# Performance work log

Measured on AMD Instinct MI355X. Metric: run time of the kernel, lower is better.

## Reference

```python
import jax, jax.numpy as jnp
import numpy as np

B, S, D, H = 4, 2048, 512, 512

def setup_inputs() -> dict:
    key = jax.random.key(0)
    ks = jax.random.split(key, 9)
    sc_d = 1.0 / np.sqrt(D)
    sc_s = 1.0 / np.sqrt(S)
    return {
        "x": jax.random.normal(ks[0], (B, S, D), dtype=jnp.float32),
        "Wq": jax.random.normal(ks[1], (D, H), dtype=jnp.float32) * sc_d,
        "bq": jnp.zeros((H,), dtype=jnp.float32),
        "Wk": jax.random.normal(ks[2], (D, H), dtype=jnp.float32) * sc_d,
        "bk": jnp.zeros((H,), dtype=jnp.float32),
        "Wv": jax.random.normal(ks[3], (D, H), dtype=jnp.float32) * sc_d,
        "bv": jnp.zeros((H,), dtype=jnp.float32),
        "Wd": jax.random.normal(ks[4], (S, H), dtype=jnp.float32) * sc_s,
        "bd": jnp.zeros((H,), dtype=jnp.float32),
    }

def reference(x, Wq, bq, Wk, bk, Wv, bv, Wd, bd):
    # q, k, v: [B, S, H]
    q = x @ Wq + bq
    k = x @ Wk + bk
    v = x @ Wv + bv
    # raw scores: [B, S, S]
    qk = jnp.einsum('bsh,bth->bst', q, k)
    # Dense+sigmoid over the last (seqlen) axis: [B, S, H]
    dense_out = jax.nn.sigmoid(qk @ Wd + bd)
    # value weights: [B, S, S]
    vw = jnp.einsum('bsh,bth->bst', dense_out, v)
    # out: [B, S, D]
    return jnp.einsum('bst,btd->bsd', vw, x)
```

## Files before the change

kernel.cpp:

```cpp
#include <hip/hip_runtime.h>
#include <hip/hip_bf16.h>
#include <stdint.h>

#define BB 4
#define SS 2048
#define DD 512
#define HH 512

typedef __attribute__((ext_vector_type(8))) short short8;
typedef __attribute__((ext_vector_type(4))) float floatx4;

typedef __attribute__((address_space(3))) uint32_t lds_u32_t;
typedef const __attribute__((address_space(1))) uint32_t glb_u32_t;

__device__ __forceinline__ void gload_lds16(const void* g, void* l) {
  __builtin_amdgcn_global_load_lds((glb_u32_t*)g, (lds_u32_t*)l, 16, 0, 0);
}

__device__ __forceinline__ short f2bf(float f) {
  __hip_bfloat16 h = __float2bfloat16(f);
  return __builtin_bit_cast(short, h);
}

__device__ __forceinline__ float bf2f(short s) {
  uint32_t u = ((uint32_t)(uint16_t)s) << 16;
  return __builtin_bit_cast(float, u);
}

template <int BM, int EPI>
__device__ __forceinline__ void gemm_core(
    const short* __restrict__ A, const short* __restrict__ Bm,
    void* __restrict__ Cm, long c_base, const float* __restrict__ bias, int K,
    int lda, int ldb, int ldc, long row0, long col0) {
  constexpr int BK = 32;
  constexpr int MF = BM / 32;
  __shared__ short As[BM * BK];
  __shared__ short Bs[128 * BK];

  const short* Ab = A + row0 * lda;
  const short* Bb = Bm + col0 * ldb;

  const int t = threadIdx.x;
  const int lane = t & 63;
  const int wid = t >> 6;
  const int wr = wid >> 1, wc = wid & 1;
  const int r16 = lane & 15;
  const int kc = (lane >> 4) * 8;

  const int st_row = t >> 2;
  const int st_k = (t & 3) * 8;

  floatx4 acc[MF][4];
#pragma unroll
  for (int i = 0; i < MF; i++)
#pragma unroll
    for (int j = 0; j < 4; j++) acc[i][j] = (floatx4)0.f;

  for (int k0 = 0; k0 < K; k0 += BK) {
#pragma unroll
    for (int i = 0; i < BM / 64; i++)
      gload_lds16(Ab + (long)(i * 64 + st_row) * lda + k0 + st_k,
                  &As[(i * 64 + st_row) * BK + st_k]);
#pragma unroll
    for (int i = 0; i < 2; i++)
      gload_lds16(Bb + (long)(i * 64 + st_row) * ldb + k0 + st_k,
                  &Bs[(i * 64 + st_row) * BK + st_k]);
    __syncthreads();

    short8 af[MF], bfr[4];
#pragma unroll
    for (int i = 0; i < MF; i++)
      af[i] = *(const short8*)&As[(wr * (BM / 2) + i * 16 + r16) * BK + kc];
#pragma unroll
    for (int j = 0; j < 4; j++)
      bfr[j] = *(const short8*)&Bs[(wc * 64 + j * 16 + r16) * BK + kc];
#pragma unroll
    for (int i = 0; i < MF; i++)
#pragma unroll
      for (int j = 0; j < 4; j++)
        acc[i][j] = __builtin_amdgcn_mfma_f32_16x16x32_bf16(af[i], bfr[j],
                                                            acc[i][j], 0, 0, 0);
    __syncthreads();
  }

#pragma unroll
  for (int i = 0; i < MF; i++) {
    const long rbase = row0 + wr * (BM / 2) + i * 16 + (lane >> 4) * 4;
#pragma unroll
    for (int j = 0; j < 4; j++) {
      const long col = col0 + wc * 64 + j * 16 + r16;
      float bv = 0.f;
      if (EPI == 1 || EPI == 2) bv = bias[col];
#pragma unroll
      for (int rg = 0; rg < 4; rg++) {
        float v = acc[i][j][rg];
        if (EPI == 1) v += bv;
        if (EPI == 2) v = 1.f / (1.f + __expf(-(v + bv)));
        const long idx = c_base + (rbase + rg) * ldc + col;
        if (EPI == 3)
          ((float*)Cm)[idx] = v;
        else
          ((__hip_bfloat16*)Cm)[idx] = __float2bfloat16(v);
      }
    }
  }
}

template <int BM, int EPI>
__global__ __launch_bounds__(256) void gemm_bt(
    const short* __restrict__ A, const short* __restrict__ Bm,
    void* __restrict__ Cm, const float* __restrict__ bias, int K, int lda,
    int ldb, int ldc, long sA, long sB, long sC) {
  const int bz = blockIdx.z;
  gemm_core<BM, EPI>(A + bz * sA, Bm + bz * sB, Cm, bz * sC, bias, K, lda, ldb,
                     ldc, (long)blockIdx.x * BM, (long)blockIdx.y * 128);
}

__global__ __launch_bounds__(256) void gemm_dual_split(
    const short* __restrict__ WdT, const short* __restrict__ kT,
    short* __restrict__ partM2, const short* __restrict__ xT,
    const short* __restrict__ vT, short* __restrict__ partM3) {
  const int bz = blockIdx.z;
  const int tb = bz >> 2, sp = bz & 3;
  const int task = tb >> 2, b = tb & 3;
  const short* A = (task ? xT + (long)b * HH * SS : WdT) + sp * 512;
  const short* B = (task ? vT : kT) + (long)b * HH * SS + sp * 512;
  short* C = (task ? partM3 : partM2) + ((long)(tb & 3) * 4 + sp) * HH * HH;
  gemm_core<128, 0>(A, B, C, 0, nullptr, 512, SS, SS, HH,
                    (long)blockIdx.x * 128, (long)blockIdx.y * 128);
}

__global__ __launch_bounds__(256) void reduce_part(
    const short* __restrict__ partM2, const short* __restrict__ partM3,
    short* __restrict__ M2, short* __restrict__ M3t) {
  const int z = blockIdx.z;
  const int b = z & 3;
  const short* src = (z < 4 ? partM2 : partM3) + (long)b * 4 * HH * HH;
  short* dst = (z < 4 ? M2 : M3t) + (long)b * HH * HH;
  const long i = ((long)blockIdx.x * 256 + threadIdx.x) * 8;
  float s[8];
#pragma unroll
  for (int j = 0; j < 8; j++) s[j] = 0.f;
#pragma unroll
  for (int sp = 0; sp < 4; sp++) {
    short8 v = *(const short8*)&src[(long)sp * HH * HH + i];
#pragma unroll
    for (int j = 0; j < 8; j++) s[j] += bf2f(v[j]);
  }
  short o[8];
#pragma unroll
  for (int j = 0; j < 8; j++) o[j] = f2bf(s[j]);
  *(short8*)&dst[i] = *(short8*)o;
}

__global__ void tr_x(const float* __restrict__ x, short* __restrict__ xb,
                     short* __restrict__ xT) {
  __shared__ float tile[32][33];
  const long b = blockIdx.z;
  const float* in = x + b * SS * DD;
  const int c0 = blockIdx.x * 32, r0 = blockIdx.y * 32;
  const int tx = threadIdx.x, ty = threadIdx.y;
#pragma unroll
  for (int i = 0; i < 32; i += 8) {
    float v = in[(long)(r0 + ty + i) * DD + c0 + tx];
    tile[ty + i][tx] = v;
    xb[(b * SS + r0 + ty + i) * DD + c0 + tx] = f2bf(v);
  }
  __syncthreads();
#pragma unroll
  for (int i = 0; i < 32; i += 8)
    xT[(b * DD + c0 + ty + i) * SS + r0 + tx] = f2bf(tile[tx][ty + i]);
}

__global__ void tr_cvt(const float* __restrict__ in, short* __restrict__ out,
                       int R, int C) {
  __shared__ float tile[32][33];
  const int c0 = blockIdx.x * 32, r0 = blockIdx.y * 32;
  const int tx = threadIdx.x, ty = threadIdx.y;
#pragma unroll
  for (int i = 0; i < 32; i += 8)
    tile[ty + i][tx] = in[(long)(r0 + ty + i) * C + c0 + tx];
  __syncthreads();
#pragma unroll
  for (int i = 0; i < 32; i += 8)
    out[(long)(c0 + ty + i) * R + r0 + tx] = f2bf(tile[tx][ty + i]);
}

__global__ void trW3(const float* __restrict__ Wq, const float* __restrict__ Wk,
                     const float* __restrict__ Wv, short* __restrict__ WT) {
  __shared__ float tile[32][33];
  const int z = blockIdx.z;
  const float* in = z == 0 ? Wq : (z == 1 ? Wk : Wv);
  short* out = WT + (long)z * HH * DD;
  const int c0 = blockIdx.x * 32, r0 = blockIdx.y * 32;
  const int tx = threadIdx.x, ty = threadIdx.y;
#pragma unroll
  for (int i = 0; i < 32; i += 8)
    tile[ty + i][tx] = in[(long)(r0 + ty + i) * HH + c0 + tx];
  __syncthreads();
#pragma unroll
  for (int i = 0; i < 32; i += 8)
    out[(long)(c0 + ty + i) * DD + r0 + tx] = f2bf(tile[tx][ty + i]);
}

__global__ void tr_kv(const short* __restrict__ qkv, short* __restrict__ kT,
                      short* __restrict__ vT) {
  __shared__ short tile[32][34];
  const int z = blockIdx.z;
  const int which = z >> 2, b = z & 3;
  const short* in = qkv + (long)b * SS * (3 * HH) + (1 + which) * HH;
  short* out = (which ? vT : kT) + (long)b * HH * SS;
  const int c0 = blockIdx.x * 32, r0 = blockIdx.y * 32;
  const int tx = threadIdx.x, ty = threadIdx.y;
#pragma unroll
  for (int i = 0; i < 32; i += 8)
    tile[ty + i][tx] = in[(long)(r0 + ty + i) * (3 * HH) + c0 + tx];
  __syncthreads();
#pragma unroll
  for (int i = 0; i < 32; i += 8)
    out[(long)(c0 + ty + i) * SS + r0 + tx] = tile[tx][ty + i];
}

__global__ void bias_cat(const float* __restrict__ bq,
                         const float* __restrict__ bk,
                         const float* __restrict__ bv,
                         float* __restrict__ bcat) {
  int i = blockIdx.x * blockDim.x + threadIdx.x;
  if (i < 512)
    bcat[i] = bq[i];
  else if (i < 1024)
    bcat[i] = bk[i - 512];
  else if (i < 1536)
    bcat[i] = bv[i - 1024];
}

extern "C" void kernel_launch(void* const* d_in, const int* in_sizes, int n_in,
                              void* d_out, int out_size, void* d_ws,
                              size_t ws_size, hipStream_t stream) {
  (void)in_sizes;
  (void)n_in;
  (void)out_size;
  (void)ws_size;
  const float* x = (const float*)d_in[0];
  const float* Wq = (const float*)d_in[1];
  const float* bq = (const float*)d_in[2];
  const float* Wk = (const float*)d_in[3];
  const float* bk = (const float*)d_in[4];
  const float* Wv = (const float*)d_in[5];
  const float* bv = (const float*)d_in[6];
  const float* Wd = (const float*)d_in[7];
  const float* bd = (const float*)d_in[8];

  char* w = (char*)d_ws;
  auto alloc = [&](size_t bytes) {
    char* p = w;
    w += (bytes + 255) & ~(size_t)255;
    return p;
  };
  short* xb = (short*)alloc((size_t)BB * SS * DD * 2);
  short* xT = (short*)alloc((size_t)BB * DD * SS * 2);
  short* WT = (short*)alloc((size_t)3 * HH * DD * 2);
  short* WdT = (short*)alloc((size_t)HH * SS * 2);
  float* bcat = (float*)alloc((size_t)3 * HH * 4);
  short* qkv = (short*)alloc((size_t)BB * SS * 3 * HH * 2);
  short* kT = (short*)alloc((size_t)BB * HH * SS * 2);
  short* vT = (short*)alloc((size_t)BB * HH * SS * 2);
  short* M2 = (short*)alloc((size_t)BB * HH * HH * 2);
  short* M3t = (short*)alloc((size_t)BB * DD * HH * 2);
  short* partM3 = (short*)alloc((size_t)BB * 4 * HH * HH * 2);
  short* partM2 = xb;
  short* dense = xb;

  dim3 tb(32, 8);
  tr_x<<<dim3(DD / 32, SS / 32, BB), tb, 0, stream>>>(x, xb, xT);
  trW3<<<dim3(HH / 32, DD / 32, 3), tb, 0, stream>>>(Wq, Wk, Wv, WT);
  tr_cvt<<<dim3(HH / 32, SS / 32, 1), tb, 0, stream>>>(Wd, WdT, SS, HH);
  bias_cat<<<6, 256, 0, stream>>>(bq, bk, bv, bcat);

  gemm_bt<128, 1><<<dim3(BB * SS / 128, 1536 / 128, 1), 256, 0, stream>>>(
      xb, WT, qkv, bcat, DD, DD, DD, 3 * HH, 0, 0, 0);
  tr_kv<<<dim3(HH / 32, SS / 32, 8), tb, 0, stream>>>(qkv, kT, vT);
  gemm_dual_split<<<dim3(4, 4, 32), 256, 0, stream>>>(WdT, kT, partM2, xT, vT,
                                                      partM3);
  reduce_part<<<dim3(128, 1, 8), 256, 0, stream>>>(partM2, partM3, M2, M3t);
  gemm_bt<64, 2><<<dim3(SS / 64, HH / 128, BB), 256, 0, stream>>>(
      qkv, M2, dense, bd, HH, 3 * HH, HH, HH, (long)SS * 3 * HH, (long)HH * HH,
      (long)SS * HH);
  gemm_bt<64, 3><<<dim3(SS / 64, DD / 128, BB), 256, 0, stream>>>(
      dense, M3t, d_out, nullptr, HH, HH, HH, DD, (long)SS * HH, (long)DD * HH,
      (long)SS * DD);
}
```

Measured before the change: 100.1 us.

## Fuse K/V transpose into QKV GEMM epilogue and merge weight prep kernels

The QKV projection now writes q row-major and writes k and v directly in transposed layout from the GEMM epilogue, which removes the separate tr_kv pass and the round trip through the qkv buffer. The three weight and bias preparation kernels are merged into one launch. The split-K GEMM switches to BM=64 tiles with twice as many blocks, and the aliased scratch buffers become separate allocations. The transposed epilogue stores are 8-byte strided writes, which may coalesce worse than the original row stores.

New measurement: 90.72 us. 9.4% less time.

```diff
diff --git a/kernel.cpp b/kernel.cpp
--- a/kernel.cpp
+++ b/kernel.cpp
@@ -27,18 +27,15 @@
   return __builtin_bit_cast(float, u);
 }
 
-template <int BM, int EPI>
-__device__ __forceinline__ void gemm_core(
-    const short* __restrict__ A, const short* __restrict__ Bm,
-    void* __restrict__ Cm, long c_base, const float* __restrict__ bias, int K,
-    int lda, int ldb, int ldc, long row0, long col0) {
+template <int BM>
+__device__ __forceinline__ void gemm_mainloop(const short* __restrict__ Ab,
+                                              const short* __restrict__ Bb,
+                                              int lda, int ldb, int K,
+                                              floatx4 (&acc)[BM / 32][4]) {
   constexpr int BK = 32;
   constexpr int MF = BM / 32;
   __shared__ short As[BM * BK];
   __shared__ short Bs[128 * BK];
-
-  const short* Ab = A + row0 * lda;
-  const short* Bb = Bm + col0 * ldb;
 
   const int t = threadIdx.x;
   const int lane = t & 63;
@@ -50,7 +47,6 @@
   const int st_row = t >> 2;
   const int st_k = (t & 3) * 8;
 
-  floatx4 acc[MF][4];
 #pragma unroll
   for (int i = 0; i < MF; i++)
 #pragma unroll
@@ -82,19 +78,28 @@
                                                             acc[i][j], 0, 0, 0);
     __syncthreads();
   }
-
-#pragma unroll
-  for (int i = 0; i < MF; i++) {
+}
+
+template <int BM, int EPI>
+__device__ __forceinline__ void epilogue_std(floatx4 (&acc)[BM / 32][4],
+                                             void* __restrict__ Cm, long c_base,
+                                             const float* __restrict__ bias,
+                                             int ldc, long row0, long col0) {
+  const int lane = threadIdx.x & 63;
+  const int wid = threadIdx.x >> 6;
+  const int wr = wid >> 1, wc = wid & 1;
+  const int r16 = lane & 15;
+#pragma unroll
+  for (int i = 0; i < BM / 32; i++) {
     const long rbase = row0 + wr * (BM / 2) + i * 16 + (lane >> 4) * 4;
 #pragma unroll
     for (int j = 0; j < 4; j++) {
       const long col = col0 + wc * 64 + j * 16 + r16;
       float bv = 0.f;
-      if (EPI == 1 || EPI == 2) bv = bias[col];
+      if (EPI == 2) bv = bias[col];
 #pragma unroll
       for (int rg = 0; rg < 4; rg++) {
         float v = acc[i][j][rg];
-        if (EPI == 1) v += bv;
         if (EPI == 2) v = 1.f / (1.f + __expf(-(v + bv)));
         const long idx = c_base + (rbase + rg) * ldc + col;
         if (EPI == 3)
@@ -112,8 +117,51 @@
     void* __restrict__ Cm, const float* __restrict__ bias, int K, int lda,
     int ldb, int ldc, long sA, long sB, long sC) {
   const int bz = blockIdx.z;
-  gemm_core<BM, EPI>(A + bz * sA, Bm + bz * sB, Cm, bz * sC, bias, K, lda, ldb,
-                     ldc, (long)blockIdx.x * BM, (long)blockIdx.y * 128);
+  floatx4 acc[BM / 32][4];
+  const long row0 = (long)blockIdx.x * BM, col0 = (long)blockIdx.y * 128;
+  gemm_mainloop<BM>(A + bz * sA + row0 * lda, Bm + bz * sB + col0 * ldb, lda,
+                    ldb, K, acc);
+  epilogue_std<BM, EPI>(acc, Cm, bz * sC, bias, ldc, row0, col0);
+}
+
+__global__ __launch_bounds__(256) void gemm_qkv(
+    const short* __restrict__ xb, const short* __restrict__ WT,
+    const float* __restrict__ bcat, short* __restrict__ q,
+    short* __restrict__ kT, short* __restrict__ vT) {
+  floatx4 acc[4][4];
+  const long row0 = (long)blockIdx.x * 128;
+  const int y = blockIdx.y;
+  gemm_mainloop<128>(xb + row0 * DD, WT + (long)y * 128 * DD, DD, DD, DD, acc);
+
+  const int lane = threadIdx.x & 63;
+  const int wid = threadIdx.x >> 6;
+  const int wr = wid >> 1, wc = wid & 1;
+  const int r16 = lane & 15;
+  const int hi4 = (lane >> 4) * 4;
+  const int mode = y >> 2;
+  const int b = (int)(row0 >> 11);
+  const int sblk = (int)(row0 & 2047);
+  short* tp = (mode == 1) ? kT : vT;
+#pragma unroll
+  for (int i = 0; i < 4; i++) {
+    const int s0 = sblk + wr * 64 + i * 16 + hi4;
+#pragma unroll
+    for (int j = 0; j < 4; j++) {
+      const int colg = y * 128 + wc * 64 + j * 16 + r16;
+      const float bv = bcat[colg];
+      short o[4];
+#pragma unroll
+      for (int rg = 0; rg < 4; rg++) o[rg] = f2bf(acc[i][j][rg] + bv);
+      if (mode == 0) {
+#pragma unroll
+        for (int rg = 0; rg < 4; rg++)
+          q[((long)b * SS + s0 + rg) * HH + colg] = o[rg];
+      } else {
+        const int cl = colg - mode * 512;
+        *(uint64_t*)&tp[((long)b * HH + cl) * SS + s0] = *(uint64_t*)o;
+      }
+    }
+  }
 }
 
 __global__ __launch_bounds__(256) void gemm_dual_split(
@@ -126,8 +174,10 @@
   const short* A = (task ? xT + (long)b * HH * SS : WdT) + sp * 512;
   const short* B = (task ? vT : kT) + (long)b * HH * SS + sp * 512;
   short* C = (task ? partM3 : partM2) + ((long)(tb & 3) * 4 + sp) * HH * HH;
-  gemm_core<128, 0>(A, B, C, 0, nullptr, 512, SS, SS, HH,
-                    (long)blockIdx.x * 128, (long)blockIdx.y * 128);
+  floatx4 acc[2][4];
+  const long row0 = (long)blockIdx.x * 64, col0 = (long)blockIdx.y * 128;
+  gemm_mainloop<64>(A + row0 * SS, B + col0 * SS, SS, SS, 512, acc);
+  epilogue_std<64, 0>(acc, C, 0, nullptr, HH, row0, col0);
 }
 
 __global__ __launch_bounds__(256) void reduce_part(
@@ -172,66 +222,43 @@
     xT[(b * DD + c0 + ty + i) * SS + r0 + tx] = f2bf(tile[tx][ty + i]);
 }
 
-__global__ void tr_cvt(const float* __restrict__ in, short* __restrict__ out,
-                       int R, int C) {
+__global__ void prep_w(const float* __restrict__ Wq,
+                       const float* __restrict__ Wk,
+                       const float* __restrict__ Wv,
+                       const float* __restrict__ Wd,
+                       const float* __restrict__ bq,
+                       const float* __restrict__ bk,
+                       const float* __restrict__ bv, short* __restrict__ WT,
+                       short* __restrict__ WdT, float* __restrict__ bcat) {
   __shared__ float tile[32][33];
-  const int c0 = blockIdx.x * 32, r0 = blockIdx.y * 32;
+  const int z = blockIdx.z, yb = blockIdx.y;
   const int tx = threadIdx.x, ty = threadIdx.y;
-#pragma unroll
-  for (int i = 0; i < 32; i += 8)
-    tile[ty + i][tx] = in[(long)(r0 + ty + i) * C + c0 + tx];
-  __syncthreads();
-#pragma unroll
-  for (int i = 0; i < 32; i += 8)
-    out[(long)(c0 + ty + i) * R + r0 + tx] = f2bf(tile[tx][ty + i]);
-}
-
-__global__ void trW3(const float* __restrict__ Wq, const float* __restrict__ Wk,
-                     const float* __restrict__ Wv, short* __restrict__ WT) {
-  __shared__ float tile[32][33];
-  const int z = blockIdx.z;
-  const float* in = z == 0 ? Wq : (z == 1 ? Wk : Wv);
-  short* out = WT + (long)z * HH * DD;
-  const int c0 = blockIdx.x * 32, r0 = blockIdx.y * 32;
-  const int tx = threadIdx.x, ty = threadIdx.y;
-#pragma unroll
-  for (int i = 0; i < 32; i += 8)
-    tile[ty + i][tx] = in[(long)(r0 + ty + i) * HH + c0 + tx];
-  __syncthreads();
-#pragma unroll
-  for (int i = 0; i < 32; i += 8)
-    out[(long)(c0 + ty + i) * DD + r0 + tx] = f2bf(tile[tx][ty + i]);
-}
-
-__global__ void tr_kv(const short* __restrict__ qkv, short* __restrict__ kT,
-                      short* __restrict__ vT) {
-  __shared__ short tile[32][34];
-  const int z = blockIdx.z;
-  const int which = z >> 2, b = z & 3;
-  const short* in = qkv + (long)b * SS * (3 * HH) + (1 + which) * HH;
-  short* out = (which ? vT : kT) + (long)b * HH * SS;
-  const int c0 = blockIdx.x * 32, r0 = blockIdx.y * 32;
-  const int tx = threadIdx.x, ty = threadIdx.y;
-#pragma unroll
-  for (int i = 0; i < 32; i += 8)
-    tile[ty + i][tx] = in[(long)(r0 + ty + i) * (3 * HH) + c0 + tx];
-  __syncthreads();
-#pragma unroll
-  for (int i = 0; i < 32; i += 8)
-    out[(long)(c0 + ty + i) * SS + r0 + tx] = tile[tx][ty + i];
-}
-
-__global__ void bias_cat(const float* __restrict__ bq,
-                         const float* __restrict__ bk,
-                         const float* __restrict__ bv,
-                         float* __restrict__ bcat) {
-  int i = blockIdx.x * blockDim.x + threadIdx.x;
-  if (i < 512)
-    bcat[i] = bq[i];
-  else if (i < 1024)
-    bcat[i] = bk[i - 512];
-  else if (i < 1536)
-    bcat[i] = bv[i - 1024];
+  if (z < 3) {
+    if (yb < 16) {
+      const float* in = z == 0 ? Wq : (z == 1 ? Wk : Wv);
+      short* out = WT + (long)z * HH * DD;
+      const int c0 = blockIdx.x * 32, r0 = yb * 32;
+#pragma unroll
+      for (int i = 0; i < 32; i += 8)
+        tile[ty + i][tx] = in[(long)(r0 + ty + i) * HH + c0 + tx];
+      __syncthreads();
+#pragma unroll
+      for (int i = 0; i < 32; i += 8)
+        out[(long)(c0 + ty + i) * DD + r0 + tx] = f2bf(tile[tx][ty + i]);
+    } else if (z == 0 && yb < 22 && blockIdx.x == 0) {
+      const int i = (yb - 16) * 256 + ty * 32 + tx;
+      bcat[i] = i < 512 ? bq[i] : (i < 1024 ? bk[i - 512] : bv[i - 1024]);
+    }
+  } else {
+    const int c0 = blockIdx.x * 32, r0 = yb * 32;
+#pragma unroll
+    for (int i = 0; i < 32; i += 8)
+      tile[ty + i][tx] = Wd[(long)(r0 + ty + i) * HH + c0 + tx];
+    __syncthreads();
+#pragma unroll
+    for (int i = 0; i < 32; i += 8)
+      WdT[(long)(c0 + ty + i) * SS + r0 + tx] = f2bf(tile[tx][ty + i]);
+  }
 }
 
 extern "C" void kernel_launch(void* const* d_in, const int* in_sizes, int n_in,
@@ -262,29 +289,27 @@
   short* WT = (short*)alloc((size_t)3 * HH * DD * 2);
   short* WdT = (short*)alloc((size_t)HH * SS * 2);
   float* bcat = (float*)alloc((size_t)3 * HH * 4);
-  short* qkv = (short*)alloc((size_t)BB * SS * 3 * HH * 2);
+  short* q = (short*)alloc((size_t)BB * SS * HH * 2);
   short* kT = (short*)alloc((size_t)BB * HH * SS * 2);
   short* vT = (short*)alloc((size_t)BB * HH * SS * 2);
+  short* partM2 = (short*)alloc((size_t)BB * 4 * HH * HH * 2);
+  short* partM3 = (short*)alloc((size_t)BB * 4 * HH * HH * 2);
   short* M2 = (short*)alloc((size_t)BB * HH * HH * 2);
   short* M3t = (short*)alloc((size_t)BB * DD * HH * 2);
-  short* partM3 = (short*)alloc((size_t)BB * 4 * HH * HH * 2);
-  short* partM2 = xb;
-  short* dense = xb;
+  short* dense = (short*)alloc((size_t)BB * SS * HH * 2);
 
   dim3 tb(32, 8);
   tr_x<<<dim3(DD / 32, SS / 32, BB), tb, 0, stream>>>(x, xb, xT);
-  trW3<<<dim3(HH / 32, DD / 32, 3), tb, 0, stream>>>(Wq, Wk, Wv, WT);
-  tr_cvt<<<dim3(HH / 32, SS / 32, 1), tb, 0, stream>>>(Wd, WdT, SS, HH);
-  bias_cat<<<6, 256, 0, stream>>>(bq, bk, bv, bcat);
-
-  gemm_bt<128, 1><<<dim3(BB * SS / 128, 1536 / 128, 1), 256, 0, stream>>>(
-      xb, WT, qkv, bcat, DD, DD, DD, 3 * HH, 0, 0, 0);
-  tr_kv<<<dim3(HH / 32, SS / 32, 8), tb, 0, stream>>>(qkv, kT, vT);
-  gemm_dual_split<<<dim3(4, 4, 32), 256, 0, stream>>>(WdT, kT, partM2, xT, vT,
+  prep_w<<<dim3(16, 64, 4), tb, 0, stream>>>(Wq, Wk, Wv, Wd, bq, bk, bv, WT,
+                                             WdT, bcat);
+
+  gemm_qkv<<<dim3(BB * SS / 128, 12, 1), 256, 0, stream>>>(xb, WT, bcat, q, kT,
+                                                           vT);
+  gemm_dual_split<<<dim3(8, 4, 32), 256, 0, stream>>>(WdT, kT, partM2, xT, vT,
                                                       partM3);
   reduce_part<<<dim3(128, 1, 8), 256, 0, stream>>>(partM2, partM3, M2, M3t);
   gemm_bt<64, 2><<<dim3(SS / 64, HH / 128, BB), 256, 0, stream>>>(
-      qkv, M2, dense, bd, HH, 3 * HH, HH, HH, (long)SS * 3 * HH, (long)HH * HH,
+      q, M2, dense, bd, HH, HH, HH, HH, (long)SS * HH, (long)HH * HH,
       (long)SS * HH);
   gemm_bt<64, 3><<<dim3(SS / 64, DD / 128, BB), 256, 0, stream>>>(
       dense, M3t, d_out, nullptr, HH, HH, HH, DD, (long)SS * HH, (long)DD * HH,
```
